# Kernel optimization log

Measured on AMD Instinct MI355X. Metric: run time of the kernel, lower is better.

The kernel has to match this reference:

```python
import jax, jax.numpy as jnp
import numpy as np

IMG = 640.0
BOX_W, OBJ_W, CLS_W = 7.5, 1.0, 0.5
EPS = 1e-7


def bce_logits(x, t):
    # numerically stable BCE-with-logits, reduction='none'
    return jnp.maximum(x, 0.0) - x * t + jnp.log1p(jnp.exp(-jnp.abs(x)))


def cxcywh_to_xyxy(b):
    cx, cy, w, h = b[..., 0], b[..., 1], b[..., 2], b[..., 3]
    return jnp.stack([cx - w / 2, cy - h / 2, cx + w / 2, cy + h / 2], axis=-1)


def ciou_elementwise(p, g):
    # p, g: (N,4) xyxy; returns CIoU per pair (diag of pairwise matrix)
    px1, py1, px2, py2 = p[:, 0], p[:, 1], p[:, 2], p[:, 3]
    gx1, gy1, gx2, gy2 = g[:, 0], g[:, 1], g[:, 2], g[:, 3]
    iw = jnp.clip(jnp.minimum(px2, gx2) - jnp.maximum(px1, gx1), 0.0)
    ih = jnp.clip(jnp.minimum(py2, gy2) - jnp.maximum(py1, gy1), 0.0)
    inter = iw * ih
    union = (px2 - px1) * (py2 - py1) + (gx2 - gx1) * (gy2 - gy1) - inter
    iou = inter / (union + EPS)
    cw = jnp.maximum(px2, gx2) - jnp.minimum(px1, gx1)
    ch = jnp.maximum(py2, gy2) - jnp.minimum(py1, gy1)
    c2 = cw * cw + ch * ch + EPS
    rho2 = ((gx1 + gx2 - px1 - px2) ** 2 + (gy1 + gy2 - py1 - py2) ** 2) / 4.0
    wp, hp = px2 - px1, py2 - py1
    wg, hg = gx2 - gx1, gy2 - gy1
    v = (4.0 / (jnp.pi ** 2)) * (jnp.arctan(wg / (hg + EPS)) - jnp.arctan(wp / (hp + EPS))) ** 2
    alpha = v / (1.0 - iou + v + EPS)
    return iou - rho2 / c2 - alpha * v


def _per_image(decoded, obj_map, cls_map, boxes, labels, min_sz, max_sz):
    # decoded (4,H,W) normalized cxcywh; obj_map (H,W); cls_map (C,H,W)
    C, H, W = cls_map.shape
    tmax = jnp.maximum(boxes[:, 2], boxes[:, 3]) * IMG
    mask = (tmax > min_sz) & (tmax <= max_sz)        # (N,)
    m = mask.astype(decoded.dtype)
    gx = jnp.clip((boxes[:, 0] * W).astype(jnp.int32), 0, W - 1)
    gy = jnp.clip((boxes[:, 1] * H).astype(jnp.int32), 0, H - 1)
    mp_box = decoded[:, gy, gx].T                    # (N,4)
    iou = jnp.clip(ciou_elementwise(cxcywh_to_xyxy(mp_box), cxcywh_to_xyxy(boxes)), -1.0, 1.0)
    box_l = jnp.sum((1.0 - iou) * m)
    mp_cls = cls_map[:, gy, gx].T                    # (N,C)
    onehot = jax.nn.one_hot(labels, C, dtype=cls_map.dtype)
    cls_l = jnp.sum(bce_logits(mp_cls, onehot) * m[:, None])
    mp_obj = obj_map[gy, gx]
    obj_pos = jnp.sum(bce_logits(mp_obj, 1.0) * m)
    # negative mask: 0 at cells hit by a valid GT, 1 elsewhere
    mask_neg = jnp.ones((H, W), obj_map.dtype).at[gy, gx].min(jnp.where(mask, 0.0, 1.0))
    neg_map = bce_logits(obj_map, 0.0)
    obj_neg = jnp.sum(neg_map * mask_neg) * 0.05
    fallback = jnp.mean(neg_map) * 0.1               # no positives at this scale for this image
    has_pos = jnp.sum(mask) > 0
    obj_l = jnp.where(has_pos, obj_pos + obj_neg, fallback)
    return jnp.where(has_pos, box_l, 0.0), obj_l, jnp.where(has_pos, cls_l, 0.0), jnp.sum(mask)


def detection_loss(p3_bbox, p3_obj, p3_cls, p4_bbox, p4_obj, p4_cls,
                   p5_bbox, p5_obj, p5_cls, boxes, labels):
    B = p3_bbox.shape[0]
    scales = [(p3_bbox, p3_obj, p3_cls, 8, 0.0, 64.0),
              (p4_bbox, p4_obj, p4_cls, 16, 64.0, 128.0),
              (p5_bbox, p5_obj, p5_cls, 32, 128.0, 10000.0)]
    tot_box = tot_obj = tot_cls = jnp.float32(0.0)
    tot_npos = jnp.int32(0)
    for reg, obj, cls, stride, min_sz, max_sz in scales:
        _, _, H, W = reg.shape
        gy, gx = jnp.meshgrid(jnp.arange(H), jnp.arange(W), indexing='ij')
        tx = jax.nn.sigmoid(reg[:, 0]); ty = jax.nn.sigmoid(reg[:, 1])
        tw = jnp.exp(reg[:, 2]); th = jnp.exp(reg[:, 3])
        decoded = jnp.stack([(gx + tx) * stride / IMG,
                             (gy + ty) * stride / IMG,
                             tw * stride / IMG,
                             th * stride / IMG], axis=1)   # (B,4,H,W)
        fn = lambda d, o, c, b, l: _per_image(d, o, c, b, l, min_sz, max_sz)
        bl, ol, cl, np_ = jax.vmap(fn)(decoded, obj[:, 0], cls, boxes, labels)
        tot_box += jnp.sum(bl); tot_obj += jnp.sum(ol); tot_cls += jnp.sum(cl)
        tot_npos += jnp.sum(np_)
    norm = jnp.maximum(tot_npos, 1).astype(tot_box.dtype)
    box_loss = tot_box / norm
    cls_loss = tot_cls / norm
    obj_loss = tot_obj / (B * 3)
    loss = BOX_W * box_loss + OBJ_W * obj_loss + CLS_W * cls_loss
    return jnp.stack([loss, box_loss, obj_loss, cls_loss])


def setup_inputs() -> dict:
    key = jax.random.key(0)
    ks = jax.random.split(key, 11)
    B, C, N = 64, 80, 60
    inp = {
        'p3_bbox': jax.random.normal(ks[0], (B, 4, 80, 80), jnp.float32),
        'p3_obj': jax.random.normal(ks[1], (B, 1, 80, 80), jnp.float32),
        'p3_cls': jax.random.normal(ks[2], (B, C, 80, 80), jnp.float32),
        'p4_bbox': jax.random.normal(ks[3], (B, 4, 40, 40), jnp.float32),
        'p4_obj': jax.random.normal(ks[4], (B, 1, 40, 40), jnp.float32),
        'p4_cls': jax.random.normal(ks[5], (B, C, 40, 40), jnp.float32),
        'p5_bbox': jax.random.normal(ks[6], (B, 4, 20, 20), jnp.float32),
        'p5_obj': jax.random.normal(ks[7], (B, 1, 20, 20), jnp.float32),
        'p5_cls': jax.random.normal(ks[8], (B, C, 20, 20), jnp.float32),
        'boxes': jax.random.uniform(ks[9], (B, N, 4), jnp.float32, 0.02, 0.98),
        'labels': jax.random.randint(ks[10], (B, N), 0, C, jnp.int32),
    }
    return inp


def reference(p3_bbox, p3_obj, p3_cls, p4_bbox, p4_obj, p4_cls,
              p5_bbox, p5_obj, p5_cls, boxes, labels):
    return detection_loss(p3_bbox, p3_obj, p3_cls, p4_bbox, p4_obj, p4_cls,
                          p5_bbox, p5_obj, p5_cls, boxes, labels)
```

## Files before the change

### kernel.cpp

```cpp
#include <hip/hip_runtime.h>
#include <math.h>

#define IMGF 640.0f
#define EPSF 1e-7f
#define NBOX 60
#define NCLS 80
#define NB   64
#define PIF  3.14159265358979323846f

__device__ __forceinline__ float bce_logits(float x, float t) {
    return fmaxf(x, 0.0f) - x * t + log1pf(expf(-fabsf(x)));
}

__device__ __forceinline__ float sigmoidf_(float x) {
    return 1.0f / (1.0f + expf(-x));
}

__device__ __forceinline__ float wave_reduce(float v) {
    #pragma unroll
    for (int o = 32; o > 0; o >>= 1) v += __shfl_down(v, o, 64);
    return v;
}

__global__ __launch_bounds__(256) void detloss_main(
    const float* __restrict__ p3b, const float* __restrict__ p3o, const float* __restrict__ p3c,
    const float* __restrict__ p4b, const float* __restrict__ p4o, const float* __restrict__ p4c,
    const float* __restrict__ p5b, const float* __restrict__ p5o, const float* __restrict__ p5c,
    const float* __restrict__ boxes, const int* __restrict__ labels,
    float* __restrict__ part)
{
    const int bid = blockIdx.x;
    const int s = bid / NB;
    const int b = bid % NB;
    const int tid = threadIdx.x;

    const float* reg; const float* obj; const float* cls;
    int H; float stridef, mn, mx;
    if (s == 0)      { reg = p3b; obj = p3o; cls = p3c; H = 80; stridef = 8.0f;  mn = 0.0f;   mx = 64.0f; }
    else if (s == 1) { reg = p4b; obj = p4o; cls = p4c; H = 40; stridef = 16.0f; mn = 64.0f;  mx = 128.0f; }
    else             { reg = p5b; obj = p5o; cls = p5c; H = 20; stridef = 32.0f; mn = 128.0f; mx = 10000.0f; }
    const int W = H, HW = H * W;
    reg += (size_t)b * 4 * HW;
    obj += (size_t)b * HW;
    cls += (size_t)b * NCLS * HW;
    const float sf = stridef / IMGF;

    __shared__ int sh_cell[NBOX];
    __shared__ int sh_lab[NBOX];
    __shared__ int sh_mask[NBOX];
    __shared__ float red[6 * 4];

    float box_p = 0.0f, objp_p = 0.0f, cls_p = 0.0f;
    float neg_p = 0.0f, sub_p = 0.0f, npos_p = 0.0f;

    if (tid < NBOX) {
        const size_t bb = ((size_t)b * NBOX + tid) * 4;
        const float bcx = boxes[bb + 0];
        const float bcy = boxes[bb + 1];
        const float bw  = boxes[bb + 2];
        const float bh  = boxes[bb + 3];
        const float tmax = fmaxf(bw, bh) * IMGF;
        const int m = (tmax > mn) && (tmax <= mx);
        int cx = (int)(bcx * (float)W); cx = min(max(cx, 0), W - 1);
        int cy = (int)(bcy * (float)H); cy = min(max(cy, 0), H - 1);
        const int cell = cy * W + cx;
        sh_cell[tid] = cell;
        sh_lab[tid]  = labels[b * NBOX + tid];
        sh_mask[tid] = m;
        if (m) {
            npos_p = 1.0f;
            const float tx = sigmoidf_(reg[0 * HW + cell]);
            const float ty = sigmoidf_(reg[1 * HW + cell]);
            const float tw = expf(reg[2 * HW + cell]);
            const float th = expf(reg[3 * HW + cell]);
            const float pcx = ((float)cx + tx) * sf;
            const float pcy = ((float)cy + ty) * sf;
            const float pw = tw * sf, ph = th * sf;
            const float px1 = pcx - pw * 0.5f, px2 = pcx + pw * 0.5f;
            const float py1 = pcy - ph * 0.5f, py2 = pcy + ph * 0.5f;
            const float qx1 = bcx - bw * 0.5f, qx2 = bcx + bw * 0.5f;
            const float qy1 = bcy - bh * 0.5f, qy2 = bcy + bh * 0.5f;
            const float iw = fmaxf(fminf(px2, qx2) - fmaxf(px1, qx1), 0.0f);
            const float ih = fmaxf(fminf(py2, qy2) - fmaxf(py1, qy1), 0.0f);
            const float inter = iw * ih;
            const float uni = (px2 - px1) * (py2 - py1) + (qx2 - qx1) * (qy2 - qy1) - inter;
            const float iou = inter / (uni + EPSF);
            const float cw = fmaxf(px2, qx2) - fminf(px1, qx1);
            const float ch = fmaxf(py2, qy2) - fminf(py1, qy1);
            const float c2 = cw * cw + ch * ch + EPSF;
            const float dx = qx1 + qx2 - px1 - px2;
            const float dy = qy1 + qy2 - py1 - py2;
            const float rho2 = (dx * dx + dy * dy) * 0.25f;
            const float wp = px2 - px1, hp = py2 - py1;
            const float wg = qx2 - qx1, hg = qy2 - qy1;
            const float da = atanf(wg / (hg + EPSF)) - atanf(wp / (hp + EPSF));
            const float v = (4.0f / (PIF * PIF)) * da * da;
            const float alpha = v / (1.0f - iou + v + EPSF);
            float ci = iou - rho2 / c2 - alpha * v;
            ci = fminf(fmaxf(ci, -1.0f), 1.0f);
            box_p  = 1.0f - ci;
            objp_p = bce_logits(obj[cell], 1.0f);
        }
    }
    __syncthreads();

    if (tid < NBOX && sh_mask[tid]) {
        const int cell = sh_cell[tid];
        bool first = true;
        for (int j = 0; j < tid; ++j)
            if (sh_mask[j] && sh_cell[j] == cell) { first = false; break; }
        if (first) sub_p = bce_logits(obj[cell], 0.0f);
    }

    for (int i = tid; i < NBOX * NCLS; i += 256) {
        const int n = i / NCLS;
        const int c = i - n * NCLS;
        if (sh_mask[n]) {
            const float x = cls[(size_t)c * HW + sh_cell[n]];
            cls_p += bce_logits(x, (c == sh_lab[n]) ? 1.0f : 0.0f);
        }
    }

    for (int i = tid; i < HW; i += 256)
        neg_p += bce_logits(obj[i], 0.0f);

    float vals[6] = { box_p, objp_p, cls_p, neg_p, sub_p, npos_p };
    const int wave = tid >> 6, lane = tid & 63;
    #pragma unroll
    for (int k = 0; k < 6; ++k) {
        const float v = wave_reduce(vals[k]);
        if (lane == 0) red[k * 4 + wave] = v;
    }
    __syncthreads();
    if (tid == 0) {
        float t[6];
        #pragma unroll
        for (int k = 0; k < 6; ++k)
            t[k] = red[k * 4 + 0] + red[k * 4 + 1] + red[k * 4 + 2] + red[k * 4 + 3];
        const bool has_pos = t[5] > 0.0f;
        const float obj_l = has_pos ? (t[1] + (t[3] - t[4]) * 0.05f)
                                    : (t[3] / (float)HW) * 0.1f;
        part[bid * 4 + 0] = has_pos ? t[0] : 0.0f;
        part[bid * 4 + 1] = obj_l;
        part[bid * 4 + 2] = has_pos ? t[2] : 0.0f;
        part[bid * 4 + 3] = t[5];
    }
}

__global__ __launch_bounds__(256) void detloss_final(
    const float* __restrict__ part, float* __restrict__ out)
{
    const int tid = threadIdx.x;
    float vb = 0.0f, vo = 0.0f, vc = 0.0f, vn = 0.0f;
    if (tid < 3 * NB) {
        vb = part[tid * 4 + 0];
        vo = part[tid * 4 + 1];
        vc = part[tid * 4 + 2];
        vn = part[tid * 4 + 3];
    }
    __shared__ float red[4 * 4];
    float vals[4] = { vb, vo, vc, vn };
    const int wave = tid >> 6, lane = tid & 63;
    #pragma unroll
    for (int k = 0; k < 4; ++k) {
        const float v = wave_reduce(vals[k]);
        if (lane == 0) red[k * 4 + wave] = v;
    }
    __syncthreads();
    if (tid == 0) {
        float t[4];
        #pragma unroll
        for (int k = 0; k < 4; ++k)
            t[k] = red[k * 4 + 0] + red[k * 4 + 1] + red[k * 4 + 2] + red[k * 4 + 3];
        const float norm = fmaxf(t[3], 1.0f);
        const float box_loss = t[0] / norm;
        const float cls_loss = t[2] / norm;
        const float obj_loss = t[1] / (float)(NB * 3);
        const float loss = 7.5f * box_loss + 1.0f * obj_loss + 0.5f * cls_loss;
        out[0] = loss;
        out[1] = box_loss;
        out[2] = obj_loss;
        out[3] = cls_loss;
    }
}

extern "C" void kernel_launch(void* const* d_in, const int* in_sizes, int n_in,
                              void* d_out, int out_size, void* d_ws, size_t ws_size,
                              hipStream_t stream) {
    const float* p3b = (const float*)d_in[0];
    const float* p3o = (const float*)d_in[1];
    const float* p3c = (const float*)d_in[2];
    const float* p4b = (const float*)d_in[3];
    const float* p4o = (const float*)d_in[4];
    const float* p4c = (const float*)d_in[5];
    const float* p5b = (const float*)d_in[6];
    const float* p5o = (const float*)d_in[7];
    const float* p5c = (const float*)d_in[8];
    const float* boxes = (const float*)d_in[9];
    const int*   labels = (const int*)d_in[10];

    float* part = (float*)d_ws;
    float* out  = (float*)d_out;

    detloss_main<<<dim3(3 * NB), dim3(256), 0, stream>>>(
        p3b, p3o, p3c, p4b, p4o, p4c, p5b, p5o, p5c, boxes, labels, part);
    detloss_final<<<dim3(1), dim3(256), 0, stream>>>(part, out);
}
```

Measured before the change: 221.0 us.

## Use fast intrinsics, 512-thread blocks, vectorized objectness sweep moved before barrier

```diff
diff --git a/kernel.cpp b/kernel.cpp
--- a/kernel.cpp
+++ b/kernel.cpp
@@ -6,14 +6,19 @@
 #define NBOX 60
 #define NCLS 80
 #define NB   64
+#define NTH  512
 #define PIF  3.14159265358979323846f
 
-__device__ __forceinline__ float bce_logits(float x, float t) {
-    return fmaxf(x, 0.0f) - x * t + log1pf(expf(-fabsf(x)));
+__device__ __forceinline__ float bce_fast(float x, float t) {
+    return fmaxf(x, 0.0f) - x * t + __logf(1.0f + __expf(-fabsf(x)));
+}
+
+__device__ __forceinline__ float bce0_fast(float x) {
+    return fmaxf(x, 0.0f) + __logf(1.0f + __expf(-fabsf(x)));
 }
 
 __device__ __forceinline__ float sigmoidf_(float x) {
-    return 1.0f / (1.0f + expf(-x));
+    return 1.0f / (1.0f + __expf(-x));
 }
 
 __device__ __forceinline__ float wave_reduce(float v) {
@@ -22,7 +27,7 @@
     return v;
 }
 
-__global__ __launch_bounds__(256) void detloss_main(
+__global__ __launch_bounds__(NTH) void detloss_main(
     const float* __restrict__ p3b, const float* __restrict__ p3o, const float* __restrict__ p3c,
     const float* __restrict__ p4b, const float* __restrict__ p4o, const float* __restrict__ p4c,
     const float* __restrict__ p5b, const float* __restrict__ p5o, const float* __restrict__ p5c,
@@ -48,7 +53,7 @@
     __shared__ int sh_cell[NBOX];
     __shared__ int sh_lab[NBOX];
     __shared__ int sh_mask[NBOX];
-    __shared__ float red[6 * 4];
+    __shared__ float red[6 * 8];
 
     float box_p = 0.0f, objp_p = 0.0f, cls_p = 0.0f;
     float neg_p = 0.0f, sub_p = 0.0f, npos_p = 0.0f;
@@ -71,8 +76,8 @@
             npos_p = 1.0f;
             const float tx = sigmoidf_(reg[0 * HW + cell]);
             const float ty = sigmoidf_(reg[1 * HW + cell]);
-            const float tw = expf(reg[2 * HW + cell]);
-            const float th = expf(reg[3 * HW + cell]);
+            const float tw = __expf(reg[2 * HW + cell]);
+            const float th = __expf(reg[3 * HW + cell]);
             const float pcx = ((float)cx + tx) * sf;
             const float pcy = ((float)cy + ty) * sf;
             const float pw = tw * sf, ph = th * sf;
@@ -99,7 +104,16 @@
             float ci = iou - rho2 / c2 - alpha * v;
             ci = fminf(fmaxf(ci, -1.0f), 1.0f);
             box_p  = 1.0f - ci;
-            objp_p = bce_logits(obj[cell], 1.0f);
+            objp_p = bce_fast(obj[cell], 1.0f);
+        }
+    }
+
+    {
+        const float4* obj4 = (const float4*)obj;
+        const int n4 = HW >> 2;
+        for (int i = tid; i < n4; i += NTH) {
+            const float4 v = obj4[i];
+            neg_p += bce0_fast(v.x) + bce0_fast(v.y) + bce0_fast(v.z) + bce0_fast(v.w);
         }
     }
     __syncthreads();
@@ -109,34 +123,36 @@
         bool first = true;
         for (int j = 0; j < tid; ++j)
             if (sh_mask[j] && sh_cell[j] == cell) { first = false; break; }
-        if (first) sub_p = bce_logits(obj[cell], 0.0f);
-    }
-
-    for (int i = tid; i < NBOX * NCLS; i += 256) {
+        if (first) sub_p = bce0_fast(obj[cell]);
+    }
+
+    #pragma unroll 2
+    for (int i = tid; i < NBOX * NCLS; i += NTH) {
         const int n = i / NCLS;
         const int c = i - n * NCLS;
         if (sh_mask[n]) {
             const float x = cls[(size_t)c * HW + sh_cell[n]];
-            cls_p += bce_logits(x, (c == sh_lab[n]) ? 1.0f : 0.0f);
-        }
-    }
-
-    for (int i = tid; i < HW; i += 256)
-        neg_p += bce_logits(obj[i], 0.0f);
+            cls_p += bce_fast(x, (c == sh_lab[n]) ? 1.0f : 0.0f);
+        }
+    }
 
     float vals[6] = { box_p, objp_p, cls_p, neg_p, sub_p, npos_p };
     const int wave = tid >> 6, lane = tid & 63;
     #pragma unroll
     for (int k = 0; k < 6; ++k) {
         const float v = wave_reduce(vals[k]);
-        if (lane == 0) red[k * 4 + wave] = v;
+        if (lane == 0) red[k * 8 + wave] = v;
     }
     __syncthreads();
     if (tid == 0) {
         float t[6];
         #pragma unroll
-        for (int k = 0; k < 6; ++k)
-            t[k] = red[k * 4 + 0] + red[k * 4 + 1] + red[k * 4 + 2] + red[k * 4 + 3];
+        for (int k = 0; k < 6; ++k) {
+            float acc = 0.0f;
+            #pragma unroll
+            for (int w = 0; w < 8; ++w) acc += red[k * 8 + w];
+            t[k] = acc;
+        }
         const bool has_pos = t[5] > 0.0f;
         const float obj_l = has_pos ? (t[1] + (t[3] - t[4]) * 0.05f)
                                     : (t[3] / (float)HW) * 0.1f;
@@ -202,7 +218,7 @@
     float* part = (float*)d_ws;
     float* out  = (float*)d_out;
 
-    detloss_main<<<dim3(3 * NB), dim3(256), 0, stream>>>(
+    detloss_main<<<dim3(3 * NB), dim3(NTH), 0, stream>>>(
         p3b, p3o, p3c, p4b, p4o, p4c, p5b, p5o, p5c, boxes, labels, part);
     detloss_final<<<dim3(1), dim3(256), 0, stream>>>(part, out);
 }
```

After: 207.6 us. -6.1%, faster.
